# Kernel optimization log

Hardware: AMD Instinct MI355X
Metric: run time of the kernel (lower is better)

The kernel has to match this reference:

```python
import jax, jax.numpy as jnp
import numpy as np

N, E, F_IN, H, D, HID, G = 50000, 800000, 64, 4, 32, 128, 1024
NEG_SLOPE = 0.2


def setup_inputs():
    key = jax.random.key(0)
    ks = jax.random.split(key, 32)
    inp = {
        "x": jax.random.normal(ks[0], (N, F_IN), dtype=jnp.float32),
        "edge_index": jax.random.randint(ks[1], (2, E), 0, N, dtype=jnp.int64),
        "batch": jnp.sort(jax.random.randint(ks[2], (N,), 0, G, dtype=jnp.int64)),
    }
    dims = [F_IN, HID, HID]
    i = 3
    for l, din in enumerate(dims):
        s = 1.0 / np.sqrt(din)
        inp[f"Wl{l}"] = jax.random.normal(ks[i], (din, H * D), dtype=jnp.float32) * s; i += 1
        inp[f"bl{l}"] = jnp.zeros((H * D,), dtype=jnp.float32)
        inp[f"Wr{l}"] = jax.random.normal(ks[i], (din, H * D), dtype=jnp.float32) * s; i += 1
        inp[f"br{l}"] = jnp.zeros((H * D,), dtype=jnp.float32)
        inp[f"att{l}"] = jax.random.normal(ks[i], (H, D), dtype=jnp.float32) * (1.0 / np.sqrt(D)); i += 1
        inp[f"b{l}"] = jnp.zeros((H * D,), dtype=jnp.float32)
    inp["Wh"] = jax.random.normal(ks[i], (HID, 1), dtype=jnp.float32) * (1.0 / np.sqrt(HID))
    inp["bh"] = jnp.zeros((1,), dtype=jnp.float32)
    return inp


def gatv2_layer(x, src, dst, Wl, bl, Wr, br, att, b):
    # GATv2Conv (eval mode, no dropout): e_ij = att . leaky_relu(Wl x_j + Wr x_i)
    xl = (x @ Wl + bl).reshape(-1, H, D)   # source transform
    xr = (x @ Wr + br).reshape(-1, H, D)   # target transform
    m = xl[src] + xr[dst]                  # [E,H,D]
    e = jnp.where(m >= 0, m, NEG_SLOPE * m)
    score = jnp.einsum("ehd,hd->eh", e, att)          # [E,H]
    smax = jax.ops.segment_max(score, dst, num_segments=N)  # [N,H]
    expv = jnp.exp(score - smax[dst])
    denom = jax.ops.segment_sum(expv, dst, num_segments=N)
    alpha = expv / denom[dst]                          # softmax over in-edges of dst
    agg = jax.ops.segment_sum(alpha[:, :, None] * xl[src], dst, num_segments=N)
    return agg.reshape(-1, H * D) + b


def reference(x, edge_index, batch, Wl0, bl0, Wr0, br0, att0, b0,
              Wl1, bl1, Wr1, br1, att1, b1,
              Wl2, bl2, Wr2, br2, att2, b2, Wh, bh):
    src, dst = edge_index[0], edge_index[1]
    params = [(Wl0, bl0, Wr0, br0, att0, b0),
              (Wl1, bl1, Wr1, br1, att1, b1),
              (Wl2, bl2, Wr2, br2, att2, b2)]
    h = x
    for p in params:
        h = gatv2_layer(h, src, dst, *p)
        h = jax.nn.elu(h)  # dropout inactive in eval
    # global mean pool over graphs
    sums = jax.ops.segment_sum(h, batch, num_segments=G)
    cnt = jax.ops.segment_sum(jnp.ones((h.shape[0],), h.dtype), batch, num_segments=G)
    pooled = sums / jnp.maximum(cnt, 1.0)[:, None]
    return pooled @ Wh + bh
```

## Files before the change

kernel.cpp:

```cpp
#include <hip/hip_runtime.h>
#include <math.h>

#define N_NODES 50000
#define N_EDGES 800000
#define HD 128
#define GG 1024
#define NEG_SLOPE 0.2f
#define SCAN_B 1024
#define NB ((N_NODES + SCAN_B - 1) / SCAN_B)

typedef __attribute__((ext_vector_type(8))) short bf16x8;
typedef __attribute__((ext_vector_type(4))) float f32x4;

__device__ __forceinline__ unsigned short f2bf(float v) {
    unsigned u = __float_as_uint(v);
    u += 0x7fff + ((u >> 16) & 1);
    return (unsigned short)(u >> 16);
}
__device__ __forceinline__ float bf2f(unsigned short s) {
    return __uint_as_float((unsigned)s << 16);
}

__global__ void convert_x(const float* __restrict__ x, unsigned short* __restrict__ Xh,
                          unsigned short* __restrict__ Xl, int total)
{
    int i = blockIdx.x * 256 + threadIdx.x;
    if (i >= total) return;
    float v = x[i];
    unsigned short hi = f2bf(v);
    unsigned short lo = f2bf(v - bf2f(hi));
    Xh[i] = hi; Xl[i] = lo;
}

__global__ void convert_w(const float* __restrict__ Wl, const float* __restrict__ Wr,
                          unsigned short* __restrict__ Wth, unsigned short* __restrict__ Wtl,
                          int K)
{
    int t = blockIdx.x * 256 + threadIdx.x;
    if (t >= 256 * K) return;
    int c = t / K, k = t - c * K;
    float v = (c < 128) ? Wl[(size_t)k * 128 + c] : Wr[(size_t)k * 128 + (c - 128)];
    unsigned short hi = f2bf(v);
    unsigned short lo = f2bf(v - bf2f(hi));
    Wth[t] = hi; Wtl[t] = lo;
}

template<int K>
__launch_bounds__(256)
__global__ void gemm_mfma(const unsigned short* __restrict__ Xh, const unsigned short* __restrict__ Xl,
                          const unsigned short* __restrict__ Wth, const unsigned short* __restrict__ Wtl,
                          const float* __restrict__ bl, const float* __restrict__ br,
                          float* __restrict__ Cl, float* __restrict__ Cr, int n)
{
    constexpr int KC = 32;
    constexpr int NCH = K / KC;
    constexpr int XR = 40;
    __shared__ unsigned short XsH[64 * XR], XsL[64 * XR];
    __shared__ unsigned short WsH[256 * XR], WsL[256 * XR];
    const int tid  = threadIdx.x;
    const int wave = tid >> 6;
    const int lane = tid & 63;
    const int quad = lane >> 4;
    const int l15  = lane & 15;
    const int row0 = blockIdx.x * 64;

    f32x4 acc[4][4];
    #pragma unroll
    for (int i = 0; i < 4; i++)
        #pragma unroll
        for (int j = 0; j < 4; j++) acc[i][j] = (f32x4){0.f, 0.f, 0.f, 0.f};

    for (int ch = 0; ch < NCH; ch++) {
        const int k0 = ch * KC;
        {
            const int r = tid >> 2, seg = tid & 3;
            const int row = row0 + r;
            const size_t go = (size_t)row * K + k0 + seg * 8;
            uint4 vh = make_uint4(0, 0, 0, 0), vl = make_uint4(0, 0, 0, 0);
            if (row < n) { vh = *(const uint4*)(Xh + go); vl = *(const uint4*)(Xl + go); }
            *(uint4*)&XsH[r * XR + seg * 8] = vh;
            *(uint4*)&XsL[r * XR + seg * 8] = vl;
        }
        #pragma unroll
        for (int i = 0; i < 4; i++) {
            const int f = tid + i * 256;
            const int wr = f >> 2, seg = f & 3;
            const size_t go = (size_t)wr * K + k0 + seg * 8;
            *(uint4*)&WsH[wr * XR + seg * 8] = *(const uint4*)(Wth + go);
            *(uint4*)&WsL[wr * XR + seg * 8] = *(const uint4*)(Wtl + go);
        }
        __syncthreads();

        bf16x8 ah[4], al[4];
        #pragma unroll
        for (int mt = 0; mt < 4; mt++) {
            ah[mt] = *(const bf16x8*)&XsH[(mt * 16 + l15) * XR + quad * 8];
            al[mt] = *(const bf16x8*)&XsL[(mt * 16 + l15) * XR + quad * 8];
        }
        #pragma unroll
        for (int nt = 0; nt < 4; nt++) {
            const int wr = wave * 64 + nt * 16 + l15;
            const bf16x8 bh = *(const bf16x8*)&WsH[wr * XR + quad * 8];
            const bf16x8 bo = *(const bf16x8*)&WsL[wr * XR + quad * 8];
            #pragma unroll
            for (int mt = 0; mt < 4; mt++) {
                acc[mt][nt] = __builtin_amdgcn_mfma_f32_16x16x32_bf16(ah[mt], bh, acc[mt][nt], 0, 0, 0);
                acc[mt][nt] = __builtin_amdgcn_mfma_f32_16x16x32_bf16(ah[mt], bo, acc[mt][nt], 0, 0, 0);
                acc[mt][nt] = __builtin_amdgcn_mfma_f32_16x16x32_bf16(al[mt], bh, acc[mt][nt], 0, 0, 0);
            }
        }
        __syncthreads();
    }

    const bool isL = (wave < 2);
    const int colbase = (wave & 1) * 64;
    const float* bias = isL ? bl : br;
    float* C = isL ? Cl : Cr;
    #pragma unroll
    for (int nt = 0; nt < 4; nt++) {
        const float bv = bias[colbase + nt * 16 + l15];
        #pragma unroll
        for (int mt = 0; mt < 4; mt++) {
            #pragma unroll
            for (int r = 0; r < 4; r++) {
                const int row = row0 + mt * 16 + quad * 4 + r;
                if (row < n)
                    C[(size_t)row * 128 + colbase + nt * 16 + l15] = acc[mt][nt][r] + bv;
            }
        }
    }
}

__global__ void deg_hist(const int* __restrict__ dst, int* __restrict__ deg) {
    int e = blockIdx.x * 256 + threadIdx.x;
    if (e < N_EDGES) atomicAdd(&deg[dst[e]], 1);
}

__launch_bounds__(SCAN_B)
__global__ void scan_block(const int* __restrict__ deg, int* __restrict__ rowptr,
                           int* __restrict__ btot)
{
    __shared__ int s[SCAN_B];
    const int tid = threadIdx.x;
    const int i = blockIdx.x * SCAN_B + tid;
    int v = (i < N_NODES) ? deg[i] : 0;
    s[tid] = v;
    __syncthreads();
    for (int off = 1; off < SCAN_B; off <<= 1) {
        int t = (tid >= off) ? s[tid - off] : 0;
        __syncthreads();
        s[tid] += t;
        __syncthreads();
    }
    if (i < N_NODES) rowptr[i] = s[tid] - v;
    if (tid == SCAN_B - 1) btot[blockIdx.x] = s[SCAN_B - 1];
}

__global__ void scan_btot(const int* __restrict__ btot, int* __restrict__ boff) {
    if (threadIdx.x == 0) {
        int a = 0;
        for (int b = 0; b < NB; b++) { boff[b] = a; a += btot[b]; }
        boff[NB] = a;
    }
}

__global__ void scan_add(const int* __restrict__ boff, int* __restrict__ rowptr,
                         int* __restrict__ cursor)
{
    int i = blockIdx.x * 256 + threadIdx.x;
    if (i < N_NODES) {
        int r = rowptr[i] + boff[i >> 10];
        rowptr[i] = r;
        cursor[i] = r;
    }
    if (i == N_NODES) rowptr[N_NODES] = boff[NB];
}

__global__ void scatter_csr(const int* __restrict__ src, const int* __restrict__ dst,
                            int* __restrict__ cursor, int* __restrict__ csr_src)
{
    int e = blockIdx.x * 256 + threadIdx.x;
    if (e >= N_EDGES) return;
    int pos = atomicAdd(&cursor[dst[e]], 1);
    csr_src[pos] = src[e];
}

__global__ void build_gptr(const int* __restrict__ batch, int* __restrict__ gptr) {
    int i = blockIdx.x * 256 + threadIdx.x;
    if (i > N_NODES) return;
    if (i == 0) {
        for (int g = 0; g <= batch[0]; g++) gptr[g] = 0;
    } else if (i == N_NODES) {
        for (int g = batch[N_NODES - 1] + 1; g <= GG; g++) gptr[g] = N_NODES;
    } else {
        int b0 = batch[i - 1], b1 = batch[i];
        for (int g = b0 + 1; g <= b1; g++) gptr[g] = i;
    }
}

__launch_bounds__(256)
__global__ void node_attn(const float* __restrict__ xl, const float* __restrict__ xr,
                          const int* __restrict__ rowptr, const int* __restrict__ csr_src,
                          const float* __restrict__ att, const float* __restrict__ bvec,
                          unsigned short* __restrict__ Hh, unsigned short* __restrict__ Hl)
{
    const int node = (blockIdx.x * 256 + threadIdx.x) >> 6;
    const int lane = threadIdx.x & 63;
    if (node >= N_NODES) return;
    const int half = lane >> 5;
    const int li   = lane & 31;

    const float4 xrd = *(const float4*)(xr + (size_t)node * HD + li * 4);
    const float4 aw  = *(const float4*)(att + li * 4);
    const int beg = rowptr[node];
    const int end = rowptr[node + 1];

    float m = -1e30f, l = 0.f;
    float4 acc = make_float4(0.f, 0.f, 0.f, 0.f);

    int e0 = beg + half;
    int s0 = (e0 < end) ? csr_src[e0] : 0;
    float4 v = *(const float4*)(xl + (size_t)s0 * HD + li * 4);

    for (int base = beg; base < end; base += 2) {
        const bool valid = (base + half) < end;
        float4 vn = v;
        if (base + 2 < end) {
            int e2 = base + 2 + half;
            int s2 = (e2 < end) ? csr_src[e2] : 0;
            vn = *(const float4*)(xl + (size_t)s2 * HD + li * 4);
        }
        float t0 = v.x + xrd.x; t0 = (t0 >= 0.f) ? t0 : NEG_SLOPE * t0;
        float t1 = v.y + xrd.y; t1 = (t1 >= 0.f) ? t1 : NEG_SLOPE * t1;
        float t2 = v.z + xrd.z; t2 = (t2 >= 0.f) ? t2 : NEG_SLOPE * t2;
        float t3 = v.w + xrd.w; t3 = (t3 >= 0.f) ? t3 : NEG_SLOPE * t3;
        float p = t0 * aw.x + t1 * aw.y + t2 * aw.z + t3 * aw.w;
        p += __shfl_xor(p, 1);
        p += __shfl_xor(p, 2);
        p += __shfl_xor(p, 4);
        const float mn = valid ? fmaxf(m, p) : m;
        const float w  = valid ? __expf(p - mn) : 0.f;
        const float sc = __expf(m - mn);
        l = l * sc + w;
        acc.x = acc.x * sc + w * v.x;
        acc.y = acc.y * sc + w * v.y;
        acc.z = acc.z * sc + w * v.z;
        acc.w = acc.w * sc + w * v.w;
        m = mn;
        v = vn;
    }

    const float mo = __shfl_xor(m, 32);
    const float lo = __shfl_xor(l, 32);
    float4 ao;
    ao.x = __shfl_xor(acc.x, 32);
    ao.y = __shfl_xor(acc.y, 32);
    ao.z = __shfl_xor(acc.z, 32);
    ao.w = __shfl_xor(acc.w, 32);
    const float mm = fmaxf(m, mo);
    const float e1 = __expf(m - mm);
    const float e2 = __expf(mo - mm);
    const float ll = l * e1 + lo * e2;
    const float inv = (ll > 0.f) ? 1.f / ll : 0.f;
    const float4 bb = *(const float4*)(bvec + li * 4);
    float o0 = (acc.x * e1 + ao.x * e2) * inv + bb.x;
    float o1 = (acc.y * e1 + ao.y * e2) * inv + bb.y;
    float o2 = (acc.z * e1 + ao.z * e2) * inv + bb.z;
    float o3 = (acc.w * e1 + ao.w * e2) * inv + bb.w;
    o0 = (o0 > 0.f) ? o0 : expm1f(o0);
    o1 = (o1 > 0.f) ? o1 : expm1f(o1);
    o2 = (o2 > 0.f) ? o2 : expm1f(o2);
    o3 = (o3 > 0.f) ? o3 : expm1f(o3);
    if (half == 0) {
        unsigned short h0 = f2bf(o0), h1 = f2bf(o1), h2 = f2bf(o2), h3 = f2bf(o3);
        unsigned short l0 = f2bf(o0 - bf2f(h0)), l1 = f2bf(o1 - bf2f(h1));
        unsigned short l2 = f2bf(o2 - bf2f(h2)), l3 = f2bf(o3 - bf2f(h3));
        *(ushort4*)(Hh + (size_t)node * HD + li * 4) = make_ushort4(h0, h1, h2, h3);
        *(ushort4*)(Hl + (size_t)node * HD + li * 4) = make_ushort4(l0, l1, l2, l3);
    }
}

__launch_bounds__(256)
__global__ void pool_head(const unsigned short* __restrict__ Hh, const unsigned short* __restrict__ Hl,
                          const int* __restrict__ gptr, const float* __restrict__ Wh,
                          const float* __restrict__ bh, float* __restrict__ out)
{
    const int g = (blockIdx.x * 256 + threadIdx.x) >> 6;
    const int lane = threadIdx.x & 63;
    if (g >= GG) return;
    const int b0 = gptr[g], b1 = gptr[g + 1];
    const float2 w = *(const float2*)(Wh + lane * 2);
    float sx = 0.f, sy = 0.f;
    for (int i = b0; i < b1; i++) {
        const unsigned vh = *(const unsigned*)(Hh + (size_t)i * HD + lane * 2);
        const unsigned vl = *(const unsigned*)(Hl + (size_t)i * HD + lane * 2);
        sx += bf2f((unsigned short)(vh & 0xffff)) + bf2f((unsigned short)(vl & 0xffff));
        sy += bf2f((unsigned short)(vh >> 16))    + bf2f((unsigned short)(vl >> 16));
    }
    float d = sx * w.x + sy * w.y;
    d += __shfl_xor(d, 1);
    d += __shfl_xor(d, 2);
    d += __shfl_xor(d, 4);
    d += __shfl_xor(d, 8);
    d += __shfl_xor(d, 16);
    d += __shfl_xor(d, 32);
    if (lane == 0) out[g] = d / fmaxf((float)(b1 - b0), 1.f) + bh[0];
}

extern "C" void kernel_launch(void* const* d_in, const int* in_sizes, int n_in,
                              void* d_out, int out_size, void* d_ws, size_t ws_size,
                              hipStream_t stream)
{
    const float* x     = (const float*)d_in[0];
    const int*   edge  = (const int*)d_in[1];
    const int*   batch = (const int*)d_in[2];
    const int*   src   = edge;
    const int*   dst   = edge + N_EDGES;
    const float* Wh    = (const float*)d_in[21];
    const float* bh    = (const float*)d_in[22];
    float* out = (float*)d_out;

    const size_t N128 = (size_t)N_NODES * HD;
    float* buf_xl = (float*)d_ws;
    float* buf_xr = buf_xl + N128;
    unsigned short* Xh  = (unsigned short*)(buf_xr + N128);
    unsigned short* Xl_ = Xh + N128;
    unsigned short* Wth = Xl_ + N128;
    unsigned short* Wtl = Wth + 3 * 256 * 128;
    int* deg     = (int*)(Wtl + 3 * 256 * 128);
    int* rowptr  = deg + N_NODES;
    int* cursor  = rowptr + N_NODES + 1;
    int* csr_src = cursor + N_NODES;
    int* btot    = csr_src + N_EDGES;
    int* boff    = btot + NB;
    int* gptr    = boff + NB + 1;

    hipMemsetAsync(deg, 0, (size_t)N_NODES * sizeof(int), stream);
    deg_hist<<<(N_EDGES + 255) / 256, 256, 0, stream>>>(dst, deg);
    scan_block<<<NB, SCAN_B, 0, stream>>>(deg, rowptr, btot);
    scan_btot<<<1, 64, 0, stream>>>(btot, boff);
    scan_add<<<(N_NODES + 256) / 256, 256, 0, stream>>>(boff, rowptr, cursor);
    scatter_csr<<<(N_EDGES + 255) / 256, 256, 0, stream>>>(src, dst, cursor, csr_src);
    build_gptr<<<(N_NODES + 256) / 256, 256, 0, stream>>>(batch, gptr);

    convert_x<<<(N_NODES * 64 + 255) / 256, 256, 0, stream>>>(x, Xh, Xl_, N_NODES * 64);
    for (int l = 0; l < 3; l++) {
        const int K = (l == 0) ? 64 : 128;
        convert_w<<<(256 * K + 255) / 256, 256, 0, stream>>>(
            (const float*)d_in[3 + 6 * l], (const float*)d_in[5 + 6 * l],
            Wth + l * 256 * 128, Wtl + l * 256 * 128, K);
    }

    const int gemm_grid = (N_NODES + 63) / 64;
    const int attn_grid = (N_NODES + 3) / 4;

    for (int l = 0; l < 3; l++) {
        const float* bl  = (const float*)d_in[4 + 6 * l];
        const float* br  = (const float*)d_in[6 + 6 * l];
        const float* att = (const float*)d_in[7 + 6 * l];
        const float* bb  = (const float*)d_in[8 + 6 * l];

        if (l == 0)
            gemm_mfma<64><<<gemm_grid, 256, 0, stream>>>(Xh, Xl_, Wth, Wtl,
                                                         bl, br, buf_xl, buf_xr, N_NODES);
        else
            gemm_mfma<128><<<gemm_grid, 256, 0, stream>>>(Xh, Xl_,
                                                          Wth + l * 256 * 128, Wtl + l * 256 * 128,
                                                          bl, br, buf_xl, buf_xr, N_NODES);
        node_attn<<<attn_grid, 256, 0, stream>>>(buf_xl, buf_xr, rowptr, csr_src,
                                                 att, bb, Xh, Xl_);
    }

    pool_head<<<GG / 4, 256, 0, stream>>>(Xh, Xl_, gptr, Wh, bh, out);
}
```

Measured before the change: 525.8 us.

## Double-buffer GEMM X tiles, read W from global, widen attention to 4 edges

The GEMM kernel now double-buffers the X tile in shared memory, prefetching the next K-chunk into registers while the MFMAs run. It reads the weight fragments directly from global or L2 instead of staging them in LDS, which shrinks LDS use and drops one barrier per chunk. The node attention kernel now handles 4 edges per wave iteration with 16 lanes per edge and 8 features per lane, and skips the online-softmax rescale when no lane raises the running max. The costs are more global weight traffic per block and heavier per-lane register use.

```diff
diff --git a/kernel.cpp b/kernel.cpp
--- a/kernel.cpp
+++ b/kernel.cpp
@@ -54,9 +54,9 @@
 {
     constexpr int KC = 32;
     constexpr int NCH = K / KC;
-    constexpr int XR = 40;
-    __shared__ unsigned short XsH[64 * XR], XsL[64 * XR];
-    __shared__ unsigned short WsH[256 * XR], WsL[256 * XR];
+    constexpr int XR = 36;
+    __shared__ unsigned short XsH[2][64 * XR];
+    __shared__ unsigned short XsL[2][64 * XR];
     const int tid  = threadIdx.x;
     const int wave = tid >> 6;
     const int lane = tid & 63;
@@ -70,44 +70,55 @@
         #pragma unroll
         for (int j = 0; j < 4; j++) acc[i][j] = (f32x4){0.f, 0.f, 0.f, 0.f};
 
+    const int sr  = tid >> 2, seg = tid & 3;
+    const int srow = row0 + sr;
+
+    {
+        uint4 vh = make_uint4(0,0,0,0), vl = make_uint4(0,0,0,0);
+        if (srow < n) {
+            const size_t go = (size_t)srow * K + seg * 8;
+            vh = *(const uint4*)(Xh + go);
+            vl = *(const uint4*)(Xl + go);
+        }
+        *(uint4*)&XsH[0][sr * XR + seg * 8] = vh;
+        *(uint4*)&XsL[0][sr * XR + seg * 8] = vl;
+    }
+    __syncthreads();
+
     for (int ch = 0; ch < NCH; ch++) {
-        const int k0 = ch * KC;
-        {
-            const int r = tid >> 2, seg = tid & 3;
-            const int row = row0 + r;
-            const size_t go = (size_t)row * K + k0 + seg * 8;
-            uint4 vh = make_uint4(0, 0, 0, 0), vl = make_uint4(0, 0, 0, 0);
-            if (row < n) { vh = *(const uint4*)(Xh + go); vl = *(const uint4*)(Xl + go); }
-            *(uint4*)&XsH[r * XR + seg * 8] = vh;
-            *(uint4*)&XsL[r * XR + seg * 8] = vl;
-        }
-        #pragma unroll
-        for (int i = 0; i < 4; i++) {
-            const int f = tid + i * 256;
-            const int wr = f >> 2, seg = f & 3;
-            const size_t go = (size_t)wr * K + k0 + seg * 8;
-            *(uint4*)&WsH[wr * XR + seg * 8] = *(const uint4*)(Wth + go);
-            *(uint4*)&WsL[wr * XR + seg * 8] = *(const uint4*)(Wtl + go);
-        }
-        __syncthreads();
-
+        const int cur = ch & 1;
+        const bool more = (ch + 1 < NCH);
+        uint4 nh = make_uint4(0,0,0,0), nl = make_uint4(0,0,0,0);
+        if (more && srow < n) {
+            const size_t go = (size_t)srow * K + (ch + 1) * KC + seg * 8;
+            nh = *(const uint4*)(Xh + go);
+            nl = *(const uint4*)(Xl + go);
+        }
+        bf16x8 bh[4], bo[4];
+        #pragma unroll
+        for (int nt = 0; nt < 4; nt++) {
+            const size_t wo = (size_t)(wave * 64 + nt * 16 + l15) * K + ch * KC + quad * 8;
+            bh[nt] = *(const bf16x8*)(Wth + wo);
+            bo[nt] = *(const bf16x8*)(Wtl + wo);
+        }
         bf16x8 ah[4], al[4];
         #pragma unroll
         for (int mt = 0; mt < 4; mt++) {
-            ah[mt] = *(const bf16x8*)&XsH[(mt * 16 + l15) * XR + quad * 8];
-            al[mt] = *(const bf16x8*)&XsL[(mt * 16 + l15) * XR + quad * 8];
+            ah[mt] = *(const bf16x8*)&XsH[cur][(mt * 16 + l15) * XR + quad * 8];
+            al[mt] = *(const bf16x8*)&XsL[cur][(mt * 16 + l15) * XR + quad * 8];
         }
         #pragma unroll
         for (int nt = 0; nt < 4; nt++) {
-            const int wr = wave * 64 + nt * 16 + l15;
-            const bf16x8 bh = *(const bf16x8*)&WsH[wr * XR + quad * 8];
-            const bf16x8 bo = *(const bf16x8*)&WsL[wr * XR + quad * 8];
             #pragma unroll
             for (int mt = 0; mt < 4; mt++) {
-                acc[mt][nt] = __builtin_amdgcn_mfma_f32_16x16x32_bf16(ah[mt], bh, acc[mt][nt], 0, 0, 0);
-                acc[mt][nt] = __builtin_amdgcn_mfma_f32_16x16x32_bf16(ah[mt], bo, acc[mt][nt], 0, 0, 0);
-                acc[mt][nt] = __builtin_amdgcn_mfma_f32_16x16x32_bf16(al[mt], bh, acc[mt][nt], 0, 0, 0);
+                acc[mt][nt] = __builtin_amdgcn_mfma_f32_16x16x32_bf16(ah[mt], bh[nt], acc[mt][nt], 0, 0, 0);
+                acc[mt][nt] = __builtin_amdgcn_mfma_f32_16x16x32_bf16(ah[mt], bo[nt], acc[mt][nt], 0, 0, 0);
+                acc[mt][nt] = __builtin_amdgcn_mfma_f32_16x16x32_bf16(al[mt], bh[nt], acc[mt][nt], 0, 0, 0);
             }
+        }
+        if (more) {
+            *(uint4*)&XsH[1 - cur][sr * XR + seg * 8] = nh;
+            *(uint4*)&XsL[1 - cur][sr * XR + seg * 8] = nl;
         }
         __syncthreads();
     }
@@ -207,76 +218,112 @@
     const int node = (blockIdx.x * 256 + threadIdx.x) >> 6;
     const int lane = threadIdx.x & 63;
     if (node >= N_NODES) return;
-    const int half = lane >> 5;
-    const int li   = lane & 31;
-
-    const float4 xrd = *(const float4*)(xr + (size_t)node * HD + li * 4);
-    const float4 aw  = *(const float4*)(att + li * 4);
+    const int eslot = lane >> 4;
+    const int li    = lane & 15;
+
+    const float* xrp = xr + (size_t)node * HD + li * 8;
+    const float4 xr0 = *(const float4*)(xrp);
+    const float4 xr1 = *(const float4*)(xrp + 4);
+    const float4 aw0 = *(const float4*)(att + li * 8);
+    const float4 aw1 = *(const float4*)(att + li * 8 + 4);
     const int beg = rowptr[node];
     const int end = rowptr[node + 1];
 
     float m = -1e30f, l = 0.f;
-    float4 acc = make_float4(0.f, 0.f, 0.f, 0.f);
-
-    int e0 = beg + half;
+    float4 a0 = make_float4(0.f, 0.f, 0.f, 0.f);
+    float4 a1 = make_float4(0.f, 0.f, 0.f, 0.f);
+
+    int e0 = beg + eslot;
     int s0 = (e0 < end) ? csr_src[e0] : 0;
-    float4 v = *(const float4*)(xl + (size_t)s0 * HD + li * 4);
-
-    for (int base = beg; base < end; base += 2) {
-        const bool valid = (base + half) < end;
-        float4 vn = v;
-        if (base + 2 < end) {
-            int e2 = base + 2 + half;
+    const float* rp0 = xl + (size_t)s0 * HD + li * 8;
+    float4 v0 = *(const float4*)(rp0);
+    float4 v1 = *(const float4*)(rp0 + 4);
+
+    for (int base = beg; base < end; base += 4) {
+        const bool valid = (base + eslot) < end;
+        float4 n0 = v0, n1 = v1;
+        if (base + 4 < end) {
+            int e2 = base + 4 + eslot;
             int s2 = (e2 < end) ? csr_src[e2] : 0;
-            vn = *(const float4*)(xl + (size_t)s2 * HD + li * 4);
-        }
-        float t0 = v.x + xrd.x; t0 = (t0 >= 0.f) ? t0 : NEG_SLOPE * t0;
-        float t1 = v.y + xrd.y; t1 = (t1 >= 0.f) ? t1 : NEG_SLOPE * t1;
-        float t2 = v.z + xrd.z; t2 = (t2 >= 0.f) ? t2 : NEG_SLOPE * t2;
-        float t3 = v.w + xrd.w; t3 = (t3 >= 0.f) ? t3 : NEG_SLOPE * t3;
-        float p = t0 * aw.x + t1 * aw.y + t2 * aw.z + t3 * aw.w;
+            const float* rp = xl + (size_t)s2 * HD + li * 8;
+            n0 = *(const float4*)(rp);
+            n1 = *(const float4*)(rp + 4);
+        }
+        float t, p;
+        t = v0.x + xr0.x; t = fmaxf(t, NEG_SLOPE * t); p  = t * aw0.x;
+        t = v0.y + xr0.y; t = fmaxf(t, NEG_SLOPE * t); p += t * aw0.y;
+        t = v0.z + xr0.z; t = fmaxf(t, NEG_SLOPE * t); p += t * aw0.z;
+        t = v0.w + xr0.w; t = fmaxf(t, NEG_SLOPE * t); p += t * aw0.w;
+        t = v1.x + xr1.x; t = fmaxf(t, NEG_SLOPE * t); p += t * aw1.x;
+        t = v1.y + xr1.y; t = fmaxf(t, NEG_SLOPE * t); p += t * aw1.y;
+        t = v1.z + xr1.z; t = fmaxf(t, NEG_SLOPE * t); p += t * aw1.z;
+        t = v1.w + xr1.w; t = fmaxf(t, NEG_SLOPE * t); p += t * aw1.w;
         p += __shfl_xor(p, 1);
         p += __shfl_xor(p, 2);
-        p += __shfl_xor(p, 4);
-        const float mn = valid ? fmaxf(m, p) : m;
-        const float w  = valid ? __expf(p - mn) : 0.f;
-        const float sc = __expf(m - mn);
-        l = l * sc + w;
-        acc.x = acc.x * sc + w * v.x;
-        acc.y = acc.y * sc + w * v.y;
-        acc.z = acc.z * sc + w * v.z;
-        acc.w = acc.w * sc + w * v.w;
-        m = mn;
-        v = vn;
-    }
-
-    const float mo = __shfl_xor(m, 32);
-    const float lo = __shfl_xor(l, 32);
-    float4 ao;
-    ao.x = __shfl_xor(acc.x, 32);
-    ao.y = __shfl_xor(acc.y, 32);
-    ao.z = __shfl_xor(acc.z, 32);
-    ao.w = __shfl_xor(acc.w, 32);
-    const float mm = fmaxf(m, mo);
-    const float e1 = __expf(m - mm);
-    const float e2 = __expf(mo - mm);
-    const float ll = l * e1 + lo * e2;
-    const float inv = (ll > 0.f) ? 1.f / ll : 0.f;
-    const float4 bb = *(const float4*)(bvec + li * 4);
-    float o0 = (acc.x * e1 + ao.x * e2) * inv + bb.x;
-    float o1 = (acc.y * e1 + ao.y * e2) * inv + bb.y;
-    float o2 = (acc.z * e1 + ao.z * e2) * inv + bb.z;
-    float o3 = (acc.w * e1 + ao.w * e2) * inv + bb.w;
-    o0 = (o0 > 0.f) ? o0 : expm1f(o0);
-    o1 = (o1 > 0.f) ? o1 : expm1f(o1);
-    o2 = (o2 > 0.f) ? o2 : expm1f(o2);
-    o3 = (o3 > 0.f) ? o3 : expm1f(o3);
-    if (half == 0) {
-        unsigned short h0 = f2bf(o0), h1 = f2bf(o1), h2 = f2bf(o2), h3 = f2bf(o3);
-        unsigned short l0 = f2bf(o0 - bf2f(h0)), l1 = f2bf(o1 - bf2f(h1));
-        unsigned short l2 = f2bf(o2 - bf2f(h2)), l3 = f2bf(o3 - bf2f(h3));
-        *(ushort4*)(Hh + (size_t)node * HD + li * 4) = make_ushort4(h0, h1, h2, h3);
-        *(ushort4*)(Hl + (size_t)node * HD + li * 4) = make_ushort4(l0, l1, l2, l3);
+
+        if (!__any(valid && (p > m))) {
+            const float w = valid ? __expf(p - m) : 0.f;
+            l += w;
+            a0.x += w * v0.x; a0.y += w * v0.y; a0.z += w * v0.z; a0.w += w * v0.w;
+            a1.x += w * v1.x; a1.y += w * v1.y; a1.z += w * v1.z; a1.w += w * v1.w;
+        } else {
+            const float mn = valid ? fmaxf(m, p) : m;
+            const float sc = __expf(m - mn);
+            const float w  = valid ? __expf(p - mn) : 0.f;
+            l = l * sc + w;
+            a0.x = a0.x * sc + w * v0.x; a0.y = a0.y * sc + w * v0.y;
+            a0.z = a0.z * sc + w * v0.z; a0.w = a0.w * sc + w * v0.w;
+            a1.x = a1.x * sc + w * v1.x; a1.y = a1.y * sc + w * v1.y;
+            a1.z = a1.z * sc + w * v1.z; a1.w = a1.w * sc + w * v1.w;
+            m = mn;
+        }
+        v0 = n0; v1 = n1;
+    }
+
+    #pragma unroll
+    for (int off = 16; off <= 32; off <<= 1) {
+        const float mo = __shfl_xor(m, off);
+        const float lo = __shfl_xor(l, off);
+        float4 b0, b1;
+        b0.x = __shfl_xor(a0.x, off); b0.y = __shfl_xor(a0.y, off);
+        b0.z = __shfl_xor(a0.z, off); b0.w = __shfl_xor(a0.w, off);
+        b1.x = __shfl_xor(a1.x, off); b1.y = __shfl_xor(a1.y, off);
+        b1.z = __shfl_xor(a1.z, off); b1.w = __shfl_xor(a1.w, off);
+        const float mm = fmaxf(m, mo);
+        const float e1 = __expf(m - mm);
+        const float e2 = __expf(mo - mm);
+        l = l * e1 + lo * e2;
+        a0.x = a0.x * e1 + b0.x * e2; a0.y = a0.y * e1 + b0.y * e2;
+        a0.z = a0.z * e1 + b0.z * e2; a0.w = a0.w * e1 + b0.w * e2;
+        a1.x = a1.x * e1 + b1.x * e2; a1.y = a1.y * e1 + b1.y * e2;
+        a1.z = a1.z * e1 + b1.z * e2; a1.w = a1.w * e1 + b1.w * e2;
+        m = mm;
+    }
+
+    if (eslot == 0) {
+        const float inv = (l > 0.f) ? 1.f / l : 0.f;
+        const float4 bb0 = *(const float4*)(bvec + li * 8);
+        const float4 bb1 = *(const float4*)(bvec + li * 8 + 4);
+        float o[8];
+        o[0] = a0.x * inv + bb0.x; o[1] = a0.y * inv + bb0.y;
+        o[2] = a0.z * inv + bb0.z; o[3] = a0.w * inv + bb0.w;
+        o[4] = a1.x * inv + bb1.x; o[5] = a1.y * inv + bb1.y;
+        o[6] = a1.z * inv + bb1.z; o[7] = a1.w * inv + bb1.w;
+        uint4 ph, pl;
+        unsigned* php = (unsigned*)&ph;
+        unsigned* plp = (unsigned*)&pl;
+        #pragma unroll
+        for (int j = 0; j < 4; j++) {
+            float u0 = o[2*j], u1 = o[2*j+1];
+            u0 = (u0 > 0.f) ? u0 : expm1f(u0);
+            u1 = (u1 > 0.f) ? u1 : expm1f(u1);
+            unsigned short h0 = f2bf(u0), h1 = f2bf(u1);
+            unsigned short q0 = f2bf(u0 - bf2f(h0)), q1 = f2bf(u1 - bf2f(h1));
+            php[j] = (unsigned)h0 | ((unsigned)h1 << 16);
+            plp[j] = (unsigned)q0 | ((unsigned)q1 << 16);
+        }
+        *(uint4*)(Hh + (size_t)node * HD + li * 8) = ph;
+        *(uint4*)(Hl + (size_t)node * HD + li * 8) = pl;
     }
 }
 
```

Result: no change. 534.6 us (+1.7%).
